# Kernel optimization log

Hardware: AMD Instinct MI355X
Metric: run time of the kernel (lower is better)

The kernel has to match this reference:

```python
import jax, jax.numpy as jnp
import numpy as np

DIM = 1024
N_HEAD = 16
HEAD_DIM = DIM // N_HEAD


def setup_inputs() -> dict:
    key = jax.random.key(0)
    ks = jax.random.split(key, 5)
    scale = 0.02
    x = jax.random.normal(ks[0], (4, 2048, DIM), dtype=jnp.float32)
    W_qkv = jax.random.normal(ks[1], (DIM, 3 * DIM), dtype=jnp.float32) * scale
    b_qkv = jnp.zeros((3 * DIM,), dtype=jnp.float32)
    W_proj = jax.random.normal(ks[2], (DIM, DIM), dtype=jnp.float32) * scale
    b_proj = jnp.zeros((DIM,), dtype=jnp.float32)
    return {"x": x, "W_qkv": W_qkv, "b_qkv": b_qkv, "W_proj": W_proj, "b_proj": b_proj}


def reference(x, W_qkv, b_qkv, W_proj, b_proj):
    B, N, C = x.shape
    qkv = x @ W_qkv + b_qkv                       # [B,N,3C]
    qkv = qkv.reshape(B, N, 3, N_HEAD, HEAD_DIM)
    q, k, v = qkv[:, :, 0], qkv[:, :, 1], qkv[:, :, 2]   # [B,N,H,d]
    # scores: [B,H,N,N]
    att = jnp.einsum('bnhd,bmhd->bhnm', q, k) * (1.0 / np.sqrt(HEAD_DIM))
    att = jax.nn.softmax(att, axis=-1)
    out = jnp.einsum('bhnm,bmhd->bnhd', att, v).reshape(B, N, C)
    return out @ W_proj + b_proj
```

## Files before the change

### kernel.cpp

```cpp
#include <hip/hip_runtime.h>
#include <stdint.h>

#define DEV __device__ __forceinline__

typedef __bf16 bf16x8 __attribute__((ext_vector_type(8)));
typedef float f32x4 __attribute__((ext_vector_type(4)));
typedef float f32x16 __attribute__((ext_vector_type(16)));

DEV uint16_t f2bf(float f) {
  union { float f; uint32_t u; } v; v.f = f;
  return (uint16_t)((v.u + 0x7FFFu + ((v.u >> 16) & 1u)) >> 16);
}
DEV float bf2f(uint16_t b) {
  union { uint32_t u; float f; } v; v.u = (uint32_t)b << 16;
  return v.f;
}

#define GLD_LDS(gsrc, ldst)                                                   \
  __builtin_amdgcn_global_load_lds(                                           \
      (__attribute__((address_space(1))) void*)(void*)(gsrc),                 \
      (__attribute__((address_space(3))) void*)(ldst), 16, 0, 0)

__global__ __launch_bounds__(256) void k_conv_x(const float* __restrict__ in,
                                                uint16_t* __restrict__ out,
                                                int n8) {
  int i = blockIdx.x * 256 + threadIdx.x;
  if (i >= n8) return;
  const float4* p = (const float4*)in;
  float4 a = p[i * 2], b = p[i * 2 + 1];
  union { uint16_t s[8]; uint4 v; } o;
  o.s[0] = f2bf(a.x); o.s[1] = f2bf(a.y); o.s[2] = f2bf(a.z); o.s[3] = f2bf(a.w);
  o.s[4] = f2bf(b.x); o.s[5] = f2bf(b.y); o.s[6] = f2bf(b.z); o.s[7] = f2bf(b.w);
  ((uint4*)out)[i] = o.v;
}

__global__ __launch_bounds__(256) void k_transpose_w(const float* __restrict__ in,
                                                     uint16_t* __restrict__ out,
                                                     int K, int Ncols) {
  __shared__ float tile[32][33];
  int n0 = blockIdx.x * 32, k0 = blockIdx.y * 32;
  int tx = threadIdx.x & 31, ty = threadIdx.x >> 5;
  #pragma unroll
  for (int r = ty; r < 32; r += 8)
    tile[r][tx] = in[(size_t)(k0 + r) * Ncols + n0 + tx];
  __syncthreads();
  #pragma unroll
  for (int r = ty; r < 32; r += 8)
    out[(size_t)(n0 + r) * K + k0 + tx] = f2bf(tile[tx][r]);
}

template <int MODE>
__global__ __launch_bounds__(256) void k_gemm(
    const uint16_t* __restrict__ A, const uint16_t* __restrict__ BT,
    const float* __restrict__ bias, float* __restrict__ fout, int Ndim,
    uint16_t* __restrict__ qb, uint16_t* __restrict__ kb,
    uint16_t* __restrict__ vtb) {
  __shared__ uint16_t As[2][128 * 32];
  __shared__ uint16_t Bs[2][128 * 32];
  const int K = 1024;
  int tid = threadIdx.x;
  int lane = tid & 63, wid = tid >> 6;
  int lg = lane >> 4, lr = lane & 15;
  int wr = wid >> 1, wc = wid & 1;
  int bm = blockIdx.x, bn = blockIdx.y;

  int c0 = tid, c1 = tid + 256;
  int r0 = c0 >> 2, sl0 = (c0 & 3) ^ (r0 & 3);
  int r1 = c1 >> 2, sl1 = (c1 & 3) ^ (r1 & 3);
  const uint16_t* gA0 = A + (size_t)(bm * 128 + r0) * K + sl0 * 8;
  const uint16_t* gA1 = A + (size_t)(bm * 128 + r1) * K + sl1 * 8;
  const uint16_t* gB0 = BT + (size_t)(bn * 128 + r0) * K + sl0 * 8;
  const uint16_t* gB1 = BT + (size_t)(bn * 128 + r1) * K + sl1 * 8;

  uint32_t aoff[4], boff[4];
  #pragma unroll
  for (int i = 0; i < 4; ++i) {
    int rowa = wr * 64 + i * 16 + lr;
    aoff[i] = rowa * 64 + ((lg ^ (rowa & 3)) << 4);
    int rowb = wc * 64 + i * 16 + lr;
    boff[i] = rowb * 64 + ((lg ^ (rowb & 3)) << 4);
  }

  f32x4 acc[4][4] = {};

  auto stageg = [&](int ks, int buf) {
    int ko = ks * 32;
    GLD_LDS(gA0 + ko, &As[buf][wid * 512]);
    GLD_LDS(gA1 + ko, &As[buf][2048 + wid * 512]);
    GLD_LDS(gB0 + ko, &Bs[buf][wid * 512]);
    GLD_LDS(gB1 + ko, &Bs[buf][2048 + wid * 512]);
  };

  auto gbody = [&](int cur, int ksn, bool dostage) {
    if (dostage) stageg(ksn, cur ^ 1);
    const char* Ab = (const char*)As + cur * 8192;
    const char* Bb = (const char*)Bs + cur * 8192;
    bf16x8 af[4], bfv[4];
    #pragma unroll
    for (int i = 0; i < 4; ++i) af[i] = *(const bf16x8*)(Ab + aoff[i]);
    #pragma unroll
    for (int j = 0; j < 4; ++j) bfv[j] = *(const bf16x8*)(Bb + boff[j]);
    __builtin_amdgcn_s_setprio(1);
    #pragma unroll
    for (int i = 0; i < 4; ++i)
      #pragma unroll
      for (int j = 0; j < 4; ++j)
        acc[i][j] = __builtin_amdgcn_mfma_f32_16x16x32_bf16(af[i], bfv[j],
                                                            acc[i][j], 0, 0, 0);
    __builtin_amdgcn_s_setprio(0);
    __syncthreads();
  };

  stageg(0, 0);
  __syncthreads();
  for (int ks = 0; ks < 30; ks += 2) {
    gbody(0, ks + 1, true);
    gbody(1, ks + 2, true);
  }
  gbody(0, 31, true);
  gbody(1, 0, false);

  int m0 = bm * 128 + wr * 64;
  int n0 = bn * 128 + wc * 64;
  if (MODE == 1) {
    #pragma unroll
    for (int i = 0; i < 4; ++i) {
      int row = m0 + i * 16 + lg * 4;
      #pragma unroll
      for (int j = 0; j < 4; ++j) {
        int col = n0 + j * 16 + lr;
        float bv = bias[col];
        #pragma unroll
        for (int r = 0; r < 4; ++r)
          fout[(size_t)(row + r) * Ndim + col] = acc[i][j][r] + bv;
      }
    }
  } else {
    #pragma unroll
    for (int i = 0; i < 4; ++i) {
      int rowb = m0 + i * 16 + lg * 4;
      int b = rowb >> 11, t = rowb & 2047;
      #pragma unroll
      for (int j = 0; j < 4; ++j) {
        int colb = n0 + j * 16 + lr;
        int which = colb >> 10;
        int hd = colb & 1023;
        int h = hd >> 6, d = hd & 63;
        float bv = bias[colb];
        size_t bh = (size_t)(b * 16 + h);
        if (which == 2) {
          union { uint16_t s[4]; uint2 v; } pk;
          #pragma unroll
          for (int r = 0; r < 4; ++r) pk.s[r] = f2bf(acc[i][j][r] + bv);
          *(uint2*)&vtb[(bh * 64 + d) * 2048 + t] = pk.v;
        } else {
          uint16_t* dst = which ? kb : qb;
          #pragma unroll
          for (int r = 0; r < 4; ++r)
            dst[(bh * 2048 + t + r) * 64 + d] = f2bf(acc[i][j][r] + bv);
        }
      }
    }
  }
}

__global__ __launch_bounds__(256) void k_attn(const uint16_t* __restrict__ qb,
                                              const uint16_t* __restrict__ kb,
                                              const uint16_t* __restrict__ vtb,
                                              uint16_t* __restrict__ ob) {
  __shared__ uint16_t SM[4][64 * 64];
  int tid = threadIdx.x, lane = tid & 63, wid = tid >> 6;
  int l31 = lane & 31, hi = lane >> 5;
  int rx = (l31 & 7) ^ (((l31 >> 3) & 3) << 1);
  int bid = blockIdx.x;
  int bh = (bid & 7) * 8 + ((bid >> 3) & 7);
  int qt = bid >> 6;
  const uint16_t* qbh = qb + (size_t)bh * 2048 * 64;
  const uint16_t* kbh = kb + (size_t)bh * 2048 * 64;
  const uint16_t* vbh = vtb + (size_t)bh * 64 * 2048;
  int q = qt * 128 + wid * 32 + l31;

  uint32_t koff[8];
  #pragma unroll
  for (int kvt = 0; kvt < 2; ++kvt)
    #pragma unroll
    for (int ks = 0; ks < 4; ++ks)
      koff[kvt * 4 + ks] = (kvt * 32 + l31) * 128 + (((ks * 2 + hi) ^ rx) << 4);

  const float QSC = 0.18033688011112042f;
  bf16x8 qf[4];
  #pragma unroll
  for (int ks = 0; ks < 4; ++ks) {
    union { uint16_t s[8]; bf16x8 v; uint4 u; } ti, to;
    ti.u = *(const uint4*)(qbh + (size_t)q * 64 + ks * 16 + hi * 8);
    #pragma unroll
    for (int e = 0; e < 8; ++e) to.s[e] = f2bf(bf2f(ti.s[e]) * QSC);
    qf[ks] = to.v;
  }

  f32x16 ovt[2] = {};
  float lrow = 0.f;

  int r0 = tid >> 3;
  int sx = (tid & 7) ^ (r0 & 7) ^ (((r0 >> 3) & 3) << 1);
  int r1 = r0 + 32;

  auto stage = [&](int kt, int buf) {
    uint16_t* KN = &SM[buf][0];
    uint16_t* VN = &SM[2 + buf][0];
    GLD_LDS(kbh + (size_t)(kt * 64 + r0) * 64 + sx * 8, KN + wid * 512);
    GLD_LDS(kbh + (size_t)(kt * 64 + r1) * 64 + sx * 8, KN + 2048 + wid * 512);
    GLD_LDS(vbh + (size_t)r0 * 2048 + kt * 64 + sx * 8, VN + wid * 512);
    GLD_LDS(vbh + (size_t)r1 * 2048 + kt * 64 + sx * 8, VN + 2048 + wid * 512);
  };

  auto body = [&](int cur, int ktn, bool dostage) {
    if (dostage) stage(ktn, cur ^ 1);
    const char* Kc = (const char*)SM + cur * 8192;
    const char* Vc = (const char*)SM + 16384 + cur * 8192;

    f32x16 sv[2] = {};
    __builtin_amdgcn_s_setprio(1);
    #pragma unroll
    for (int kvt = 0; kvt < 2; ++kvt)
      #pragma unroll
      for (int ks = 0; ks < 4; ++ks) {
        bf16x8 kf = *(const bf16x8*)(Kc + koff[kvt * 4 + ks]);
        sv[kvt] = __builtin_amdgcn_mfma_f32_32x32x16_bf16(kf, qf[ks], sv[kvt], 0, 0, 0);
      }
    __builtin_amdgcn_s_setprio(0);

    float ps0 = 0.f, ps1 = 0.f, ps2 = 0.f, ps3 = 0.f;
    #pragma unroll
    for (int t = 0; t < 2; ++t)
      #pragma unroll
      for (int r = 0; r < 16; r += 4) {
        float p0 = __builtin_amdgcn_exp2f(sv[t][r + 0]);
        float p1 = __builtin_amdgcn_exp2f(sv[t][r + 1]);
        float p2 = __builtin_amdgcn_exp2f(sv[t][r + 2]);
        float p3 = __builtin_amdgcn_exp2f(sv[t][r + 3]);
        sv[t][r + 0] = p0; sv[t][r + 1] = p1;
        sv[t][r + 2] = p2; sv[t][r + 3] = p3;
        ps0 += p0; ps1 += p1; ps2 += p2; ps3 += p3;
      }
    lrow += (ps0 + ps1) + (ps2 + ps3);

    union PB { uint32_t w[4]; bf16x8 v; } pb[4];
    #pragma unroll
    for (int t = 0; t < 2; ++t)
      #pragma unroll
      for (int s = 0; s < 2; ++s) {
        int rb = s * 8;
        #pragma unroll
        for (int i = 0; i < 2; ++i) {
          uint32_t a, b;
          asm("v_cvt_pk_bf16_f32 %0, %1, %2"
              : "=v"(a) : "v"(sv[t][rb + 2 * i]), "v"(sv[t][rb + 2 * i + 1]));
          asm("v_cvt_pk_bf16_f32 %0, %1, %2"
              : "=v"(b) : "v"(sv[t][rb + 4 + 2 * i]), "v"(sv[t][rb + 4 + 2 * i + 1]));
          asm("v_permlane32_swap_b32 %0, %1" : "+v"(a), "+v"(b));
          pb[2 * t + s].w[i] = a;
          pb[2 * t + s].w[2 + i] = b;
        }
      }

    __builtin_amdgcn_s_setprio(1);
    #pragma unroll
    for (int dt = 0; dt < 2; ++dt)
      #pragma unroll
      for (int ks = 0; ks < 4; ++ks) {
        bf16x8 vf = *(const bf16x8*)(Vc + koff[dt * 4 + ks]);
        ovt[dt] = __builtin_amdgcn_mfma_f32_32x32x16_bf16(vf, pb[ks].v, ovt[dt], 0, 0, 0);
      }
    __builtin_amdgcn_s_setprio(0);

    __syncthreads();
  };

  stage(0, 0);
  __syncthreads();
  for (int t = 0; t < 30; t += 2) {
    body(0, t + 1, true);
    body(1, t + 2, true);
  }
  body(0, 31, true);
  body(1, 0, false);

  lrow += __shfl_xor(lrow, 32);
  float inv = 1.f / lrow;
  int b = bh >> 4, h = bh & 15;
  size_t base = ((size_t)b * 2048 + q) * 1024 + h * 64;
  #pragma unroll
  for (int dt = 0; dt < 2; ++dt)
    #pragma unroll
    for (int r = 0; r < 16; r += 2) {
      int d = dt * 32 + (r & 3) + 8 * (r >> 2) + 4 * hi;
      uint32_t w = (uint32_t)f2bf(ovt[dt][r] * inv) |
                   ((uint32_t)f2bf(ovt[dt][r + 1] * inv) << 16);
      *(uint32_t*)&ob[base + d] = w;
    }
}

extern "C" void kernel_launch(void* const* d_in, const int* in_sizes, int n_in,
                              void* d_out, int out_size, void* d_ws,
                              size_t ws_size, hipStream_t stream) {
  const float* x = (const float*)d_in[0];
  const float* Wqkv = (const float*)d_in[1];
  const float* bqkv = (const float*)d_in[2];
  const float* Wproj = (const float*)d_in[3];
  const float* bproj = (const float*)d_in[4];
  float* out = (float*)d_out;
  char* ws = (char*)d_ws;

  uint16_t* xb = (uint16_t*)(ws);
  uint16_t* wqkvt = (uint16_t*)(ws + (16ull << 20));
  uint16_t* wprojt = (uint16_t*)(ws + (22ull << 20));
  uint16_t* qbuf = (uint16_t*)(ws + (24ull << 20));
  uint16_t* kbuf = (uint16_t*)(ws + (40ull << 20));
  uint16_t* vtb = (uint16_t*)(ws + (56ull << 20));
  uint16_t* ob = xb;

  k_conv_x<<<4096, 256, 0, stream>>>(x, xb, 1048576);
  k_transpose_w<<<dim3(96, 32), 256, 0, stream>>>(Wqkv, wqkvt, 1024, 3072);
  k_transpose_w<<<dim3(32, 32), 256, 0, stream>>>(Wproj, wprojt, 1024, 1024);
  k_gemm<0><<<dim3(64, 24), 256, 0, stream>>>(xb, wqkvt, bqkv, nullptr, 3072,
                                              qbuf, kbuf, vtb);
  k_attn<<<1024, 256, 0, stream>>>(qbuf, kbuf, vtb, ob);
  k_gemm<1><<<dim3(64, 8), 256, 0, stream>>>(ob, wprojt, bproj, out, 1024,
                                             nullptr, nullptr, nullptr);
}
```

Measured before the change: 201.6 us.

## Fuse prep kernels, remap GEMM blocks, fold Q scaling into QKV epilogue

```diff
diff --git a/kernel.cpp b/kernel.cpp
--- a/kernel.cpp
+++ b/kernel.cpp
@@ -4,6 +4,7 @@
 #define DEV __device__ __forceinline__
 
 typedef __bf16 bf16x8 __attribute__((ext_vector_type(8)));
+typedef float f32x2 __attribute__((ext_vector_type(2)));
 typedef float f32x4 __attribute__((ext_vector_type(4)));
 typedef float f32x16 __attribute__((ext_vector_type(16)));
 
@@ -11,9 +12,11 @@
   union { float f; uint32_t u; } v; v.f = f;
   return (uint16_t)((v.u + 0x7FFFu + ((v.u >> 16) & 1u)) >> 16);
 }
-DEV float bf2f(uint16_t b) {
-  union { uint32_t u; float f; } v; v.u = (uint32_t)b << 16;
-  return v.f;
+
+DEV f32x2 pkadd(f32x2 a, f32x2 b) {
+  f32x2 d;
+  asm("v_pk_add_f32 %0, %1, %2" : "=v"(d) : "v"(a), "v"(b));
+  return d;
 }
 
 #define GLD_LDS(gsrc, ldst)                                                   \
@@ -21,24 +24,36 @@
       (__attribute__((address_space(1))) void*)(void*)(gsrc),                 \
       (__attribute__((address_space(3))) void*)(ldst), 16, 0, 0)
 
-__global__ __launch_bounds__(256) void k_conv_x(const float* __restrict__ in,
-                                                uint16_t* __restrict__ out,
-                                                int n8) {
-  int i = blockIdx.x * 256 + threadIdx.x;
-  if (i >= n8) return;
-  const float4* p = (const float4*)in;
-  float4 a = p[i * 2], b = p[i * 2 + 1];
-  union { uint16_t s[8]; uint4 v; } o;
-  o.s[0] = f2bf(a.x); o.s[1] = f2bf(a.y); o.s[2] = f2bf(a.z); o.s[3] = f2bf(a.w);
-  o.s[4] = f2bf(b.x); o.s[5] = f2bf(b.y); o.s[6] = f2bf(b.z); o.s[7] = f2bf(b.w);
-  ((uint4*)out)[i] = o.v;
-}
-
-__global__ __launch_bounds__(256) void k_transpose_w(const float* __restrict__ in,
-                                                     uint16_t* __restrict__ out,
-                                                     int K, int Ncols) {
+__global__ __launch_bounds__(256) void k_prep(const float* __restrict__ x,
+                                              const float* __restrict__ Wqkv,
+                                              const float* __restrict__ Wproj,
+                                              uint16_t* __restrict__ xb,
+                                              uint16_t* __restrict__ wqkvt,
+                                              uint16_t* __restrict__ wprojt) {
   __shared__ float tile[32][33];
-  int n0 = blockIdx.x * 32, k0 = blockIdx.y * 32;
+  int bid = blockIdx.x;
+  if (bid < 4096) {
+    int i = bid * 256 + threadIdx.x;
+    const float4* p = (const float4*)x;
+    float4 a = p[i * 2], b = p[i * 2 + 1];
+    union { uint16_t s[8]; uint4 v; } o;
+    o.s[0] = f2bf(a.x); o.s[1] = f2bf(a.y); o.s[2] = f2bf(a.z); o.s[3] = f2bf(a.w);
+    o.s[4] = f2bf(b.x); o.s[5] = f2bf(b.y); o.s[6] = f2bf(b.z); o.s[7] = f2bf(b.w);
+    ((uint4*)xb)[i] = o.v;
+    return;
+  }
+  const float* in;
+  uint16_t* out;
+  int n0, k0, Ncols;
+  if (bid < 7168) {
+    int local = bid - 4096;
+    in = Wqkv; out = wqkvt; Ncols = 3072;
+    n0 = (local % 96) * 32; k0 = (local / 96) * 32;
+  } else {
+    int local = bid - 7168;
+    in = Wproj; out = wprojt; Ncols = 1024;
+    n0 = (local % 32) * 32; k0 = (local / 32) * 32;
+  }
   int tx = threadIdx.x & 31, ty = threadIdx.x >> 5;
   #pragma unroll
   for (int r = ty; r < 32; r += 8)
@@ -46,10 +61,10 @@
   __syncthreads();
   #pragma unroll
   for (int r = ty; r < 32; r += 8)
-    out[(size_t)(n0 + r) * K + k0 + tx] = f2bf(tile[tx][r]);
-}
-
-template <int MODE>
+    out[(size_t)(n0 + r) * 1024 + k0 + tx] = f2bf(tile[tx][r]);
+}
+
+template <int MODE, int GRIDN>
 __global__ __launch_bounds__(256) void k_gemm(
     const uint16_t* __restrict__ A, const uint16_t* __restrict__ BT,
     const float* __restrict__ bias, float* __restrict__ fout, int Ndim,
@@ -62,7 +77,9 @@
   int lane = tid & 63, wid = tid >> 6;
   int lg = lane >> 4, lr = lane & 15;
   int wr = wid >> 1, wc = wid & 1;
-  int bm = blockIdx.x, bn = blockIdx.y;
+  int bid = blockIdx.x;
+  int lin = (bid & 7) * (64 * GRIDN / 8) + (bid >> 3);
+  int bm = lin % 64, bn = lin / 64;
 
   int c0 = tid, c1 = tid + 256;
   int r0 = c0 >> 2, sl0 = (c0 & 3) ^ (r0 & 3);
@@ -83,16 +100,16 @@
 
   f32x4 acc[4][4] = {};
 
-  auto stageg = [&](int ks, int buf) {
-    int ko = ks * 32;
-    GLD_LDS(gA0 + ko, &As[buf][wid * 512]);
-    GLD_LDS(gA1 + ko, &As[buf][2048 + wid * 512]);
-    GLD_LDS(gB0 + ko, &Bs[buf][wid * 512]);
-    GLD_LDS(gB1 + ko, &Bs[buf][2048 + wid * 512]);
+  auto stageg = [&](int buf) {
+    GLD_LDS(gA0, &As[buf][wid * 512]);
+    GLD_LDS(gA1, &As[buf][2048 + wid * 512]);
+    GLD_LDS(gB0, &Bs[buf][wid * 512]);
+    GLD_LDS(gB1, &Bs[buf][2048 + wid * 512]);
+    gA0 += 32; gA1 += 32; gB0 += 32; gB1 += 32;
   };
 
-  auto gbody = [&](int cur, int ksn, bool dostage) {
-    if (dostage) stageg(ksn, cur ^ 1);
+  auto gbody = [&](int cur, bool dostage) {
+    if (dostage) stageg(cur ^ 1);
     const char* Ab = (const char*)As + cur * 8192;
     const char* Bb = (const char*)Bs + cur * 8192;
     bf16x8 af[4], bfv[4];
@@ -111,14 +128,14 @@
     __syncthreads();
   };
 
-  stageg(0, 0);
+  stageg(0);
   __syncthreads();
   for (int ks = 0; ks < 30; ks += 2) {
-    gbody(0, ks + 1, true);
-    gbody(1, ks + 2, true);
-  }
-  gbody(0, 31, true);
-  gbody(1, 0, false);
+    gbody(0, true);
+    gbody(1, true);
+  }
+  gbody(0, true);
+  gbody(1, false);
 
   int m0 = bm * 128 + wr * 64;
   int n0 = bn * 128 + wc * 64;
@@ -136,6 +153,7 @@
       }
     }
   } else {
+    const float QSC = 0.18033688011112042f;
     #pragma unroll
     for (int i = 0; i < 4; ++i) {
       int rowb = m0 + i * 16 + lg * 4;
@@ -155,9 +173,10 @@
           *(uint2*)&vtb[(bh * 64 + d) * 2048 + t] = pk.v;
         } else {
           uint16_t* dst = which ? kb : qb;
+          float sc = which ? 1.f : QSC;
           #pragma unroll
           for (int r = 0; r < 4; ++r)
-            dst[(bh * 2048 + t + r) * 64 + d] = f2bf(acc[i][j][r] + bv);
+            dst[(bh * 2048 + t + r) * 64 + d] = f2bf((acc[i][j][r] + bv) * sc);
         }
       }
     }
@@ -187,35 +206,33 @@
     for (int ks = 0; ks < 4; ++ks)
       koff[kvt * 4 + ks] = (kvt * 32 + l31) * 128 + (((ks * 2 + hi) ^ rx) << 4);
 
-  const float QSC = 0.18033688011112042f;
   bf16x8 qf[4];
   #pragma unroll
-  for (int ks = 0; ks < 4; ++ks) {
-    union { uint16_t s[8]; bf16x8 v; uint4 u; } ti, to;
-    ti.u = *(const uint4*)(qbh + (size_t)q * 64 + ks * 16 + hi * 8);
-    #pragma unroll
-    for (int e = 0; e < 8; ++e) to.s[e] = f2bf(bf2f(ti.s[e]) * QSC);
-    qf[ks] = to.v;
-  }
+  for (int ks = 0; ks < 4; ++ks)
+    qf[ks] = *(const bf16x8*)(qbh + (size_t)q * 64 + ks * 16 + hi * 8);
 
   f32x16 ovt[2] = {};
-  float lrow = 0.f;
+  f32x2 lr2 = {0.f, 0.f};
 
   int r0 = tid >> 3;
   int sx = (tid & 7) ^ (r0 & 7) ^ (((r0 >> 3) & 3) << 1);
-  int r1 = r0 + 32;
-
-  auto stage = [&](int kt, int buf) {
+  const uint16_t* kp0 = kbh + (size_t)r0 * 64 + sx * 8;
+  const uint16_t* kp1 = kbh + (size_t)(r0 + 32) * 64 + sx * 8;
+  const uint16_t* vp0 = vbh + (size_t)r0 * 2048 + sx * 8;
+  const uint16_t* vp1 = vbh + (size_t)(r0 + 32) * 2048 + sx * 8;
+
+  auto stage = [&](int buf) {
     uint16_t* KN = &SM[buf][0];
     uint16_t* VN = &SM[2 + buf][0];
-    GLD_LDS(kbh + (size_t)(kt * 64 + r0) * 64 + sx * 8, KN + wid * 512);
-    GLD_LDS(kbh + (size_t)(kt * 64 + r1) * 64 + sx * 8, KN + 2048 + wid * 512);
-    GLD_LDS(vbh + (size_t)r0 * 2048 + kt * 64 + sx * 8, VN + wid * 512);
-    GLD_LDS(vbh + (size_t)r1 * 2048 + kt * 64 + sx * 8, VN + 2048 + wid * 512);
+    GLD_LDS(kp0, KN + wid * 512);
+    GLD_LDS(kp1, KN + 2048 + wid * 512);
+    GLD_LDS(vp0, VN + wid * 512);
+    GLD_LDS(vp1, VN + 2048 + wid * 512);
+    kp0 += 4096; kp1 += 4096; vp0 += 64; vp1 += 64;
   };
 
-  auto body = [&](int cur, int ktn, bool dostage) {
-    if (dostage) stage(ktn, cur ^ 1);
+  auto body = [&](int cur, bool dostage) {
+    if (dostage) stage(cur ^ 1);
     const char* Kc = (const char*)SM + cur * 8192;
     const char* Vc = (const char*)SM + 16384 + cur * 8192;
 
@@ -230,20 +247,18 @@
       }
     __builtin_amdgcn_s_setprio(0);
 
-    float ps0 = 0.f, ps1 = 0.f, ps2 = 0.f, ps3 = 0.f;
     #pragma unroll
     for (int t = 0; t < 2; ++t)
       #pragma unroll
-      for (int r = 0; r < 16; r += 4) {
-        float p0 = __builtin_amdgcn_exp2f(sv[t][r + 0]);
-        float p1 = __builtin_amdgcn_exp2f(sv[t][r + 1]);
-        float p2 = __builtin_amdgcn_exp2f(sv[t][r + 2]);
-        float p3 = __builtin_amdgcn_exp2f(sv[t][r + 3]);
-        sv[t][r + 0] = p0; sv[t][r + 1] = p1;
-        sv[t][r + 2] = p2; sv[t][r + 3] = p3;
-        ps0 += p0; ps1 += p1; ps2 += p2; ps3 += p3;
-      }
-    lrow += (ps0 + ps1) + (ps2 + ps3);
+      for (int r = 0; r < 16; ++r) sv[t][r] = __builtin_amdgcn_exp2f(sv[t][r]);
+
+    #define SVP(t, i) __builtin_shufflevector(sv[t], sv[t], 2 * (i), 2 * (i) + 1)
+    f32x2 s0 = pkadd(pkadd(pkadd(SVP(0, 0), SVP(0, 1)), pkadd(SVP(0, 2), SVP(0, 3))),
+                     pkadd(pkadd(SVP(0, 4), SVP(0, 5)), pkadd(SVP(0, 6), SVP(0, 7))));
+    f32x2 s1 = pkadd(pkadd(pkadd(SVP(1, 0), SVP(1, 1)), pkadd(SVP(1, 2), SVP(1, 3))),
+                     pkadd(pkadd(SVP(1, 4), SVP(1, 5)), pkadd(SVP(1, 6), SVP(1, 7))));
+    #undef SVP
+    lr2 = pkadd(lr2, pkadd(s0, s1));
 
     union PB { uint32_t w[4]; bf16x8 v; } pb[4];
     #pragma unroll
@@ -277,15 +292,16 @@
     __syncthreads();
   };
 
-  stage(0, 0);
+  stage(0);
   __syncthreads();
   for (int t = 0; t < 30; t += 2) {
-    body(0, t + 1, true);
-    body(1, t + 2, true);
-  }
-  body(0, 31, true);
-  body(1, 0, false);
-
+    body(0, true);
+    body(1, true);
+  }
+  body(0, true);
+  body(1, false);
+
+  float lrow = lr2.x + lr2.y;
   lrow += __shfl_xor(lrow, 32);
   float inv = 1.f / lrow;
   int b = bh >> 4, h = bh & 15;
@@ -320,12 +336,10 @@
   uint16_t* vtb = (uint16_t*)(ws + (56ull << 20));
   uint16_t* ob = xb;
 
-  k_conv_x<<<4096, 256, 0, stream>>>(x, xb, 1048576);
-  k_transpose_w<<<dim3(96, 32), 256, 0, stream>>>(Wqkv, wqkvt, 1024, 3072);
-  k_transpose_w<<<dim3(32, 32), 256, 0, stream>>>(Wproj, wprojt, 1024, 1024);
-  k_gemm<0><<<dim3(64, 24), 256, 0, stream>>>(xb, wqkvt, bqkv, nullptr, 3072,
-                                              qbuf, kbuf, vtb);
+  k_prep<<<8192, 256, 0, stream>>>(x, Wqkv, Wproj, xb, wqkvt, wprojt);
+  k_gemm<0, 24><<<1536, 256, 0, stream>>>(xb, wqkvt, bqkv, nullptr, 3072,
+                                          qbuf, kbuf, vtb);
   k_attn<<<1024, 256, 0, stream>>>(qbuf, kbuf, vtb, ob);
-  k_gemm<1><<<dim3(64, 8), 256, 0, stream>>>(ob, wprojt, bproj, out, 1024,
-                                             nullptr, nullptr, nullptr);
-}
+  k_gemm<1, 8><<<512, 256, 0, stream>>>(ob, wprojt, bproj, out, 1024,
+                                        nullptr, nullptr, nullptr);
+}
```

New measurement: 211.8 us. 5.1% more time.
